# Kernel tuning notes

Hardware: AMD Instinct MI355X
Metric: run time of the kernel (lower is better)

The kernel has to match this reference:

```python
import jax, jax.numpy as jnp
import numpy as np

EMBED = 1024
HEADS = 16
HEAD_DIM = EMBED // HEADS


def setup_inputs() -> dict:
    key = jax.random.key(0)
    ks = jax.random.split(key, 8)
    N, S = 4, 2048
    scale = 1.0 / np.sqrt(HEAD_DIM)
    return {
        "values": jax.random.normal(ks[0], (N, S, EMBED), jnp.float32),
        "keys": jax.random.normal(ks[1], (N, S, EMBED), jnp.float32),
        "query": jax.random.normal(ks[2], (N, S, EMBED), jnp.float32),
        "Wv": jax.random.normal(ks[3], (HEAD_DIM, HEAD_DIM), jnp.float32) * scale,
        "Wk": jax.random.normal(ks[4], (HEAD_DIM, HEAD_DIM), jnp.float32) * scale,
        "Wq": jax.random.normal(ks[5], (HEAD_DIM, HEAD_DIM), jnp.float32) * scale,
        "Wo": jax.random.normal(ks[6], (EMBED, EMBED), jnp.float32) / np.sqrt(EMBED),
        "bo": jax.random.normal(ks[7], (EMBED,), jnp.float32) * 0.01,
    }


def reference(values, keys, query, Wv, Wk, Wq, Wo, bo):
    N = query.shape[0]
    # reshape to [N, S, H, D]
    v = values.reshape(N, -1, HEADS, HEAD_DIM)
    k = keys.reshape(N, -1, HEADS, HEAD_DIM)
    q = query.reshape(N, -1, HEADS, HEAD_DIM)
    # per-head linear projections (torch Linear: x @ W.T)
    v = jnp.einsum("nshd,ed->nshe", v, Wv)
    k = jnp.einsum("nshd,ed->nshe", k, Wk)
    q = jnp.einsum("nshd,ed->nshe", q, Wq)
    # full attention matrix [N, H, Q, K]; note scale uses embed_size**0.5 as in source
    energy = jnp.einsum("nqhd,nkhd->nhqk", q, k)
    attn = jax.nn.softmax(energy / jnp.sqrt(jnp.asarray(EMBED, energy.dtype)), axis=3)
    out = jnp.einsum("nhql,nlhd->nqhd", attn, v).reshape(N, -1, EMBED)
    return out @ Wo.T + bo
```

## Files before the change

### kernel.cpp

```cpp
#include <hip/hip_runtime.h>
#include <hip/hip_bf16.h>

#define EMBED 1024
#define HEADS 16
#define HD    64
#define NB    4
#define SEQ   2048

typedef __bf16 bf16x2 __attribute__((ext_vector_type(2)));
typedef __bf16 bf16x8 __attribute__((ext_vector_type(8)));
typedef float  f32x4  __attribute__((ext_vector_type(4)));
typedef float  f32x16 __attribute__((ext_vector_type(16)));
typedef unsigned uint2v __attribute__((ext_vector_type(2)));

__device__ __forceinline__ unsigned short f2bf(float f) {
    union { float f; unsigned u; } v; v.f = f;
    unsigned r = v.u + 0x7fffu + ((v.u >> 16) & 1u);
    return (unsigned short)(r >> 16);
}
__device__ __forceinline__ unsigned pack2(float a, float b) {
#if __has_builtin(__builtin_amdgcn_cvt_pk_bf16_f32)
    union { bf16x2 v; unsigned u; } c;
    c.v = __builtin_amdgcn_cvt_pk_bf16_f32(a, b);
    return c.u;
#else
    return (unsigned)f2bf(a) | ((unsigned)f2bf(b) << 16);
#endif
}

__global__ __launch_bounds__(256) void cvt_kernel(const float* __restrict__ src,
                                                  unsigned* __restrict__ dst) {
    int i = blockIdx.x * 256 + threadIdx.x;
    float4 v = ((const float4*)src)[i];
    uint2 o;
    o.x = pack2(v.x, v.y);
    o.y = pack2(v.z, v.w);
    ((uint2*)dst)[i] = o;
}

__global__ __launch_bounds__(256) void proj_kernel(
    const float* __restrict__ xq, const float* __restrict__ xk, const float* __restrict__ xv,
    const float* __restrict__ Wq, const float* __restrict__ Wk, const float* __restrict__ Wv,
    unsigned short* __restrict__ Qp, unsigned short* __restrict__ Kp, unsigned short* __restrict__ Vt)
{
    __shared__ __align__(16) unsigned short Wl[64 * 72];
    __shared__ __align__(16) unsigned short Xl[256 * 72];

    int bx = blockIdx.x;
    int p  = bx >> 9;
    int r  = bx & 511;
    int st = r & 7, h = (r >> 3) & 15, n = r >> 7;
    int s0 = st * 256;

    const float* x = (p == 0) ? xq : (p == 1) ? xk : xv;
    const float* W = (p == 0) ? Wq : (p == 1) ? Wk : Wv;
    const float sc = (p == 0) ? 0.045084220027780106f : 1.0f;

    int tid = threadIdx.x;

    for (int i = 0; i < 4; ++i) {
        int idx = tid + i * 256;
        int row = idx >> 4, c4 = idx & 15;
        float4 wv = ((const float4*)W)[row * 16 + c4];
        uint2 pw;
        pw.x = pack2(wv.x, wv.y);
        pw.y = pack2(wv.z, wv.w);
        *(uint2*)&Wl[row * 72 + c4 * 4] = pw;
    }
    const float* xbase = x + (size_t)(n * SEQ + s0) * EMBED + h * HD;
    for (int i = 0; i < 16; ++i) {
        int idx = tid + i * 256;
        int row = idx >> 4, c4 = idx & 15;
        float4 v = *(const float4*)(xbase + (size_t)row * EMBED + c4 * 4);
        uint2 px;
        px.x = pack2(v.x, v.y);
        px.y = pack2(v.z, v.w);
        *(uint2*)&Xl[row * 72 + c4 * 4] = px;
    }
    __syncthreads();

    int w = tid >> 6, lane = tid & 63, ln = lane & 15, qd = lane >> 4;

    bf16x8 a[4][2], b[4][2];
#pragma unroll
    for (int mt = 0; mt < 4; ++mt)
#pragma unroll
        for (int kt = 0; kt < 2; ++kt)
            a[mt][kt] = *(const bf16x8*)&Xl[(w * 64 + mt * 16 + ln) * 72 + kt * 32 + qd * 8];
#pragma unroll
    for (int i = 0; i < 4; ++i)
#pragma unroll
        for (int kt = 0; kt < 2; ++kt)
            b[i][kt] = *(const bf16x8*)&Wl[(i * 16 + ln) * 72 + kt * 32 + qd * 8];

    f32x4 acc[4][4];
    const f32x4 fz = {0.f, 0.f, 0.f, 0.f};
#pragma unroll
    for (int i = 0; i < 4; ++i)
#pragma unroll
        for (int j = 0; j < 4; ++j) acc[i][j] = fz;

    if (p < 2) {
#pragma unroll
        for (int i = 0; i < 4; ++i)
#pragma unroll
            for (int j = 0; j < 4; ++j) {
                acc[i][j] = __builtin_amdgcn_mfma_f32_16x16x32_bf16(b[i][0], a[j][0], acc[i][j], 0, 0, 0);
                acc[i][j] = __builtin_amdgcn_mfma_f32_16x16x32_bf16(b[i][1], a[j][1], acc[i][j], 0, 0, 0);
            }
#pragma unroll
        for (int i = 0; i < 4; ++i)
#pragma unroll
            for (int j = 0; j < 4; ++j) {
                uint2 pk;
                pk.x = pack2(acc[i][j][0] * sc, acc[i][j][1] * sc);
                pk.y = pack2(acc[i][j][2] * sc, acc[i][j][3] * sc);
                *(uint2*)&Xl[(w * 64 + j * 16 + ln) * 72 + i * 16 + qd * 4] = pk;
            }
        __syncthreads();
        unsigned short* outp = (p == 0 ? Qp : Kp) + (size_t)(n * HEADS + h) * SEQ * HD + (size_t)s0 * HD;
        for (int i = 0; i < 8; ++i) {
            int idx = tid + i * 256;
            int row = idx >> 3, ch = idx & 7;
            *(uint4*)(outp + (size_t)row * HD + ch * 8) = *(const uint4*)&Xl[row * 72 + ch * 8];
        }
    } else {
#pragma unroll
        for (int mt = 0; mt < 4; ++mt)
#pragma unroll
            for (int i = 0; i < 4; ++i) {
                acc[mt][i] = __builtin_amdgcn_mfma_f32_16x16x32_bf16(a[mt][0], b[i][0], acc[mt][i], 0, 0, 0);
                acc[mt][i] = __builtin_amdgcn_mfma_f32_16x16x32_bf16(a[mt][1], b[i][1], acc[mt][i], 0, 0, 0);
            }
        __syncthreads();
#pragma unroll
        for (int mt = 0; mt < 4; ++mt)
#pragma unroll
            for (int i = 0; i < 4; ++i) {
                uint2 pk;
                pk.x = pack2(acc[mt][i][0], acc[mt][i][1]);
                pk.y = pack2(acc[mt][i][2], acc[mt][i][3]);
                *(uint2*)&Xl[(i * 16 + ln) * 264 + w * 64 + mt * 16 + qd * 4] = pk;
            }
        __syncthreads();
        unsigned short* outp = Vt + (size_t)(n * HEADS + h) * HD * SEQ + s0;
        for (int i = 0; i < 8; ++i) {
            int idx = tid + i * 256;
            int row = idx >> 5, ch = idx & 31;
            *(uint4*)(outp + (size_t)row * SEQ + ch * 8) = *(const uint4*)&Xl[row * 264 + ch * 8];
        }
    }
}

__global__ __launch_bounds__(512, 4) void attn_kernel(
    const unsigned short* __restrict__ Qp, const unsigned short* __restrict__ Kp,
    const unsigned short* __restrict__ Vt, unsigned short* __restrict__ Xattn)
{
    __shared__ __align__(16) unsigned short SMEM[18432];
    unsigned short* Kl = SMEM;
    unsigned short* Vl = SMEM + 9216;

    int bx = blockIdx.x;
    int head = bx >> 3, qt = bx & 7;
    int n = head >> 4, h16 = head & 15;
    int q0 = qt * 256;

    int tid = threadIdx.x;
    int w = tid >> 6, lane = tid & 63;
    int qc = lane & 31, hh = lane >> 5;

    const unsigned short* Qb = Qp + (size_t)head * SEQ * HD;
    const unsigned short* Kb = Kp + (size_t)head * SEQ * HD;
    const unsigned short* Vb = Vt + (size_t)head * HD * SEQ;

    bf16x8 qb[4];
    {
        int qrow = q0 + w * 32 + qc;
#pragma unroll
        for (int kk = 0; kk < 4; ++kk)
            qb[kk] = *(const bf16x8*)(Qb + (size_t)qrow * HD + kk * 16 + hh * 8);
    }

    f32x16 ot0, ot1;
#pragma unroll
    for (int i = 0; i < 16; ++i) { ot0[i] = 0.f; ot1[i] = 0.f; }
    float ls[4] = {0.f, 0.f, 0.f, 0.f};

    int srow = tid >> 3, sch = tid & 7;

    uint4 rK, rV;
    rK = *(const uint4*)(Kb + (size_t)srow * HD + sch * 8);
    rV = *(const uint4*)(Vb + (size_t)srow * SEQ + 0 + sch * 8);
    *(uint4*)&Kl[srow * 72 + sch * 8] = rK;
    *(uint4*)&Vl[srow * 72 + sch * 8] = rV;
    rK = *(const uint4*)(Kb + (size_t)(64 + srow) * HD + sch * 8);
    rV = *(const uint4*)(Vb + (size_t)srow * SEQ + 64 + sch * 8);

    for (int kc = 0; kc < SEQ; kc += 64) {
        int cur = (kc >> 6) & 1, nxt = cur ^ 1;
        int curo = cur * 4608;
        __syncthreads();

        unsigned pk[2][8];
#pragma unroll
        for (int kt = 0; kt < 2; ++kt) {
            f32x16 c;
#pragma unroll
            for (int i = 0; i < 16; ++i) c[i] = 0.f;
            __builtin_amdgcn_s_setprio(1);
#pragma unroll
            for (int kk = 0; kk < 4; ++kk) {
                bf16x8 ka = *(const bf16x8*)&Kl[curo + (kt * 32 + qc) * 72 + kk * 16 + hh * 8];
                c = __builtin_amdgcn_mfma_f32_32x32x16_bf16(ka, qb[kk], c, 0, 0, 0);
            }
            __builtin_amdgcn_s_setprio(0);
#pragma unroll
            for (int i = 0; i < 8; ++i) {
                float p0 = __builtin_amdgcn_exp2f(c[2 * i]);
                float p1 = __builtin_amdgcn_exp2f(c[2 * i + 1]);
                ls[i & 3] += p0 + p1;
                pk[kt][i] = pack2(p0, p1);
            }
        }

        if (kc + 64 < SEQ) {
            *(uint4*)&Kl[nxt * 4608 + srow * 72 + sch * 8] = rK;
            *(uint4*)&Vl[nxt * 4608 + srow * 72 + sch * 8] = rV;
            int kn = kc + 128 <= SEQ - 64 ? kc + 128 : SEQ - 64;
            rK = *(const uint4*)(Kb + (size_t)(kn + srow) * HD + sch * 8);
            rV = *(const uint4*)(Vb + (size_t)srow * SEQ + kn + sch * 8);
        }

        __builtin_amdgcn_s_setprio(1);
#pragma unroll
        for (int g = 0; g < 4; ++g) {
            const unsigned* P = pk[g >> 1];
            int base = (g & 1) * 4;
            union { unsigned u[4]; bf16x8 v; } bb;
#if __has_builtin(__builtin_amdgcn_permlane32_swap)
            uint2v r  = __builtin_amdgcn_permlane32_swap(P[base + 0], P[base + 2], false, false);
            uint2v rr = __builtin_amdgcn_permlane32_swap(P[base + 1], P[base + 3], false, false);
            bb.u[0] = r.x;
            bb.u[1] = rr.x;
            bb.u[2] = r.y;
            bb.u[3] = rr.y;
#else
            unsigned s0 = hh ? P[base + 0] : P[base + 2];
            unsigned s1 = hh ? P[base + 1] : P[base + 3];
            unsigned r0 = (unsigned)__shfl_xor((int)s0, 32);
            unsigned r1 = (unsigned)__shfl_xor((int)s1, 32);
            bb.u[0] = hh ? r0 : P[base + 0];
            bb.u[1] = hh ? r1 : P[base + 1];
            bb.u[2] = hh ? P[base + 2] : r0;
            bb.u[3] = hh ? P[base + 3] : r1;
#endif
            bf16x8 va0 = *(const bf16x8*)&Vl[curo + qc * 72 + g * 16 + hh * 8];
            bf16x8 va1 = *(const bf16x8*)&Vl[curo + (32 + qc) * 72 + g * 16 + hh * 8];
            ot0 = __builtin_amdgcn_mfma_f32_32x32x16_bf16(va0, bb.v, ot0, 0, 0, 0);
            ot1 = __builtin_amdgcn_mfma_f32_32x32x16_bf16(va1, bb.v, ot1, 0, 0, 0);
        }
        __builtin_amdgcn_s_setprio(0);
    }

    float lsum = (ls[0] + ls[1]) + (ls[2] + ls[3]);
    lsum += __shfl_xor(lsum, 32);
    float inv = 1.0f / lsum;

    __syncthreads();
    int qlocal = w * 32 + qc;
#pragma unroll
    for (int dt = 0; dt < 2; ++dt) {
        const f32x16& o = dt ? ot1 : ot0;
#pragma unroll
        for (int g = 0; g < 4; ++g) {
            uint2 p;
            p.x = pack2(o[4 * g + 0] * inv, o[4 * g + 1] * inv);
            p.y = pack2(o[4 * g + 2] * inv, o[4 * g + 3] * inv);
            *(uint2*)&SMEM[qlocal * 72 + dt * 32 + g * 8 + hh * 4] = p;
        }
    }
    __syncthreads();
    unsigned short* ob = Xattn + (size_t)(n * SEQ + q0) * EMBED + h16 * HD;
#pragma unroll
    for (int i = 0; i < 4; ++i) {
        int idx = tid + i * 512;
        int row = idx >> 3, ch = idx & 7;
        *(uint4*)(ob + (size_t)row * EMBED + ch * 8) = *(const uint4*)&SMEM[row * 72 + ch * 8];
    }
}

__global__ __launch_bounds__(256, 4) void outproj_kernel(
    const unsigned short* __restrict__ X, const unsigned short* __restrict__ Wb,
    const float* __restrict__ bo, float* __restrict__ out)
{
    __shared__ __align__(16) unsigned short Al[64 * 72];
    __shared__ __align__(16) unsigned short Bl[128 * 72];

    int bx = blockIdx.x;
    int cm = bx >> 3, cn = bx & 7;
    int m0 = cm * 64, c0 = cn * 128;
    int tid = threadIdx.x;
    int w = tid >> 6, lane = tid & 63, ln = lane & 15, qd = lane >> 4;
    int chw = w * 32;

    f32x4 acc[4][2];
    const f32x4 fz = {0.f, 0.f, 0.f, 0.f};
#pragma unroll
    for (int mt = 0; mt < 4; ++mt)
#pragma unroll
        for (int nt = 0; nt < 2; ++nt) acc[mt][nt] = fz;

    for (int k0 = 0; k0 < EMBED; k0 += 64) {
        {
#pragma unroll
            for (int i = 0; i < 2; ++i) {
                int idx = tid + i * 256;
                int r2 = idx >> 3, c2 = idx & 7;
                uint4 av = *(const uint4*)(X + (size_t)(m0 + r2) * EMBED + k0 + c2 * 8);
                *(uint4*)&Al[r2 * 72 + c2 * 8] = av;
            }
#pragma unroll
            for (int i = 0; i < 4; ++i) {
                int idx = tid + i * 256;
                int r2 = idx >> 3, c2 = idx & 7;
                uint4 bv = *(const uint4*)(Wb + (size_t)(c0 + r2) * EMBED + k0 + c2 * 8);
                *(uint4*)&Bl[r2 * 72 + c2 * 8] = bv;
            }
        }
        __syncthreads();
        bf16x8 af[4][2], bf_[2][2];
#pragma unroll
        for (int mt = 0; mt < 4; ++mt)
#pragma unroll
            for (int kt = 0; kt < 2; ++kt)
                af[mt][kt] = *(const bf16x8*)&Al[(mt * 16 + ln) * 72 + kt * 32 + qd * 8];
#pragma unroll
        for (int nt = 0; nt < 2; ++nt)
#pragma unroll
            for (int kt = 0; kt < 2; ++kt)
                bf_[nt][kt] = *(const bf16x8*)&Bl[(chw + nt * 16 + ln) * 72 + kt * 32 + qd * 8];
#pragma unroll
        for (int mt = 0; mt < 4; ++mt)
#pragma unroll
            for (int nt = 0; nt < 2; ++nt) {
                acc[mt][nt] = __builtin_amdgcn_mfma_f32_16x16x32_bf16(af[mt][0], bf_[nt][0], acc[mt][nt], 0, 0, 0);
                acc[mt][nt] = __builtin_amdgcn_mfma_f32_16x16x32_bf16(af[mt][1], bf_[nt][1], acc[mt][nt], 0, 0, 0);
            }
        __syncthreads();
    }

#pragma unroll
    for (int nt = 0; nt < 2; ++nt) {
        int col = c0 + chw + nt * 16 + ln;
        float bias = bo[col];
#pragma unroll
        for (int mt = 0; mt < 4; ++mt) {
            int row = m0 + mt * 16 + qd * 4;
#pragma unroll
            for (int rg = 0; rg < 4; ++rg)
                out[(size_t)(row + rg) * EMBED + col] = acc[mt][nt][rg] + bias;
        }
    }
}

extern "C" void kernel_launch(void* const* d_in, const int* in_sizes, int n_in,
                              void* d_out, int out_size, void* d_ws, size_t ws_size,
                              hipStream_t stream) {
    const float* values = (const float*)d_in[0];
    const float* keys   = (const float*)d_in[1];
    const float* query  = (const float*)d_in[2];
    const float* Wv     = (const float*)d_in[3];
    const float* Wk     = (const float*)d_in[4];
    const float* Wq     = (const float*)d_in[5];
    const float* Wo     = (const float*)d_in[6];
    const float* bo     = (const float*)d_in[7];
    float* out = (float*)d_out;

    unsigned short* ws = (unsigned short*)d_ws;
    const size_t HSZ = (size_t)NB * HEADS * SEQ * HD;
    unsigned short* Qp = ws;
    unsigned short* Kp = Qp + HSZ;
    unsigned short* Vt = Kp + HSZ;
    unsigned short* Xa = Vt + HSZ;
    unsigned short* Wb = Xa + HSZ;

    cvt_kernel<<<1024, 256, 0, stream>>>(Wo, (unsigned*)Wb);
    proj_kernel<<<1536, 256, 0, stream>>>(query, keys, values, Wq, Wk, Wv, Qp, Kp, Vt);
    attn_kernel<<<512, 512, 0, stream>>>(Qp, Kp, Vt, Xa);
    outproj_kernel<<<1024, 256, 0, stream>>>(Xa, Wb, bo, out);
}
```

Measured before the change: 264.4 us.

## Software-pipeline attention loop: overlap QK of next tile with PV of previous

Restructures the attention main loop into a three-buffer LDS ring so that the QK^T MFMAs and softmax exp for tile i run in the same iteration as the PV MFMAs for tile i-1. The aim is to let exp/pack work overlap with matrix-core work and to remove the per-tile dependency stall between softmax and PV. It also replaces __syncthreads with a custom barrier that waits only on LDS counters, so in-flight global prefetch loads are not drained at each barrier. LDS grows from 36 KB to 54 KB per block, which may reduce occupancy, and more live registers (two score accumulators plus the packed P fragments) raise register pressure.

```diff
diff --git a/kernel.cpp b/kernel.cpp
--- a/kernel.cpp
+++ b/kernel.cpp
@@ -26,6 +26,12 @@
 #else
     return (unsigned)f2bf(a) | ((unsigned)f2bf(b) << 16);
 #endif
+}
+
+__device__ __forceinline__ void sync_lds() {
+    asm volatile("s_waitcnt lgkmcnt(0)" ::: "memory");
+    __builtin_amdgcn_s_barrier();
+    asm volatile("" ::: "memory");
 }
 
 __global__ __launch_bounds__(256) void cvt_kernel(const float* __restrict__ src,
@@ -156,9 +162,7 @@
     const unsigned short* __restrict__ Qp, const unsigned short* __restrict__ Kp,
     const unsigned short* __restrict__ Vt, unsigned short* __restrict__ Xattn)
 {
-    __shared__ __align__(16) unsigned short SMEM[18432];
-    unsigned short* Kl = SMEM;
-    unsigned short* Vl = SMEM + 9216;
+    __shared__ __align__(16) unsigned short SMEM[27648];
 
     int bx = blockIdx.x;
     int head = bx >> 3, qt = bx & 7;
@@ -187,80 +191,118 @@
     float ls[4] = {0.f, 0.f, 0.f, 0.f};
 
     int srow = tid >> 3, sch = tid & 7;
+    int soff = srow * 72 + sch * 8;
+
+    unsigned pkP[16];
+    f32x16 c0, c1;
+
+#define QK_STEP(KBASE)  do {                                                    \
+    _Pragma("unroll")                                                           \
+    for (int _i = 0; _i < 16; ++_i) { c0[_i] = 0.f; c1[_i] = 0.f; }             \
+    __builtin_amdgcn_s_setprio(1);                                              \
+    _Pragma("unroll")                                                           \
+    for (int kk = 0; kk < 4; ++kk) {                                            \
+        bf16x8 ka = *(const bf16x8*)&SMEM[(KBASE) + qc * 72 + kk * 16 + hh * 8];\
+        c0 = __builtin_amdgcn_mfma_f32_32x32x16_bf16(ka, qb[kk], c0, 0, 0, 0);  \
+    }                                                                           \
+    _Pragma("unroll")                                                           \
+    for (int kk = 0; kk < 4; ++kk) {                                            \
+        bf16x8 ka = *(const bf16x8*)&SMEM[(KBASE) + (32 + qc) * 72 + kk * 16 + hh * 8]; \
+        c1 = __builtin_amdgcn_mfma_f32_32x32x16_bf16(ka, qb[kk], c1, 0, 0, 0);  \
+    }                                                                           \
+    __builtin_amdgcn_s_setprio(0);                                              \
+} while (0)
+
+#define SOFTMAX_STEP() do {                                                     \
+    _Pragma("unroll")                                                           \
+    for (int _i = 0; _i < 8; ++_i) {                                            \
+        float p0 = __builtin_amdgcn_exp2f(c0[2 * _i]);                          \
+        float p1 = __builtin_amdgcn_exp2f(c0[2 * _i + 1]);                      \
+        ls[_i & 3] += p0 + p1;                                                  \
+        pkP[_i] = pack2(p0, p1);                                                \
+    }                                                                           \
+    _Pragma("unroll")                                                           \
+    for (int _i = 0; _i < 8; ++_i) {                                            \
+        float p0 = __builtin_amdgcn_exp2f(c1[2 * _i]);                          \
+        float p1 = __builtin_amdgcn_exp2f(c1[2 * _i + 1]);                      \
+        ls[_i & 3] += p0 + p1;                                                  \
+        pkP[8 + _i] = pack2(p0, p1);                                            \
+    }                                                                           \
+} while (0)
+
+#if __has_builtin(__builtin_amdgcn_permlane32_swap)
+#define PV_FRAG(P, BASE, BB) do {                                               \
+    uint2v r  = __builtin_amdgcn_permlane32_swap((P)[(BASE) + 0], (P)[(BASE) + 2], false, false); \
+    uint2v rr = __builtin_amdgcn_permlane32_swap((P)[(BASE) + 1], (P)[(BASE) + 3], false, false); \
+    BB.u[0] = r.x; BB.u[1] = rr.x; BB.u[2] = r.y; BB.u[3] = rr.y;               \
+} while (0)
+#else
+#define PV_FRAG(P, BASE, BB) do {                                               \
+    unsigned s0_ = hh ? (P)[(BASE) + 0] : (P)[(BASE) + 2];                      \
+    unsigned s1_ = hh ? (P)[(BASE) + 1] : (P)[(BASE) + 3];                      \
+    unsigned r0_ = (unsigned)__shfl_xor((int)s0_, 32);                          \
+    unsigned r1_ = (unsigned)__shfl_xor((int)s1_, 32);                          \
+    BB.u[0] = hh ? r0_ : (P)[(BASE) + 0];                                       \
+    BB.u[1] = hh ? r1_ : (P)[(BASE) + 1];                                       \
+    BB.u[2] = hh ? (P)[(BASE) + 2] : r0_;                                       \
+    BB.u[3] = hh ? (P)[(BASE) + 3] : r1_;                                       \
+} while (0)
+#endif
+
+#define PV_STEP(VBASE) do {                                                     \
+    __builtin_amdgcn_s_setprio(1);                                              \
+    _Pragma("unroll")                                                           \
+    for (int g = 0; g < 4; ++g) {                                               \
+        union { unsigned u[4]; bf16x8 v; } bb;                                  \
+        PV_FRAG(pkP, (g >> 1) * 8 + (g & 1) * 4, bb);                           \
+        bf16x8 va0 = *(const bf16x8*)&SMEM[(VBASE) + qc * 72 + g * 16 + hh * 8];        \
+        bf16x8 va1 = *(const bf16x8*)&SMEM[(VBASE) + (32 + qc) * 72 + g * 16 + hh * 8]; \
+        ot0 = __builtin_amdgcn_mfma_f32_32x32x16_bf16(va0, bb.v, ot0, 0, 0, 0); \
+        ot1 = __builtin_amdgcn_mfma_f32_32x32x16_bf16(va1, bb.v, ot1, 0, 0, 0); \
+    }                                                                           \
+    __builtin_amdgcn_s_setprio(0);                                              \
+} while (0)
 
     uint4 rK, rV;
     rK = *(const uint4*)(Kb + (size_t)srow * HD + sch * 8);
     rV = *(const uint4*)(Vb + (size_t)srow * SEQ + 0 + sch * 8);
-    *(uint4*)&Kl[srow * 72 + sch * 8] = rK;
-    *(uint4*)&Vl[srow * 72 + sch * 8] = rV;
+    *(uint4*)&SMEM[0 + soff] = rK;
+    *(uint4*)&SMEM[4608 + soff] = rV;
     rK = *(const uint4*)(Kb + (size_t)(64 + srow) * HD + sch * 8);
     rV = *(const uint4*)(Vb + (size_t)srow * SEQ + 64 + sch * 8);
 
-    for (int kc = 0; kc < SEQ; kc += 64) {
-        int cur = (kc >> 6) & 1, nxt = cur ^ 1;
-        int curo = cur * 4608;
-        __syncthreads();
-
-        unsigned pk[2][8];
-#pragma unroll
-        for (int kt = 0; kt < 2; ++kt) {
-            f32x16 c;
-#pragma unroll
-            for (int i = 0; i < 16; ++i) c[i] = 0.f;
-            __builtin_amdgcn_s_setprio(1);
-#pragma unroll
-            for (int kk = 0; kk < 4; ++kk) {
-                bf16x8 ka = *(const bf16x8*)&Kl[curo + (kt * 32 + qc) * 72 + kk * 16 + hh * 8];
-                c = __builtin_amdgcn_mfma_f32_32x32x16_bf16(ka, qb[kk], c, 0, 0, 0);
-            }
-            __builtin_amdgcn_s_setprio(0);
-#pragma unroll
-            for (int i = 0; i < 8; ++i) {
-                float p0 = __builtin_amdgcn_exp2f(c[2 * i]);
-                float p1 = __builtin_amdgcn_exp2f(c[2 * i + 1]);
-                ls[i & 3] += p0 + p1;
-                pk[kt][i] = pack2(p0, p1);
-            }
-        }
-
-        if (kc + 64 < SEQ) {
-            *(uint4*)&Kl[nxt * 4608 + srow * 72 + sch * 8] = rK;
-            *(uint4*)&Vl[nxt * 4608 + srow * 72 + sch * 8] = rV;
-            int kn = kc + 128 <= SEQ - 64 ? kc + 128 : SEQ - 64;
+    sync_lds();
+    QK_STEP(0);
+    *(uint4*)&SMEM[9216 + soff] = rK;
+    *(uint4*)&SMEM[9216 + 4608 + soff] = rV;
+    rK = *(const uint4*)(Kb + (size_t)(128 + srow) * HD + sch * 8);
+    rV = *(const uint4*)(Vb + (size_t)srow * SEQ + 128 + sch * 8);
+    SOFTMAX_STEP();
+
+    int b_prv = 0, b_cur = 9216, b_nxt = 18432;
+
+    for (int i = 1; i < 32; ++i) {
+        sync_lds();
+        QK_STEP(b_cur);
+        if (i < 31) {
+            *(uint4*)&SMEM[b_nxt + soff] = rK;
+            *(uint4*)&SMEM[b_nxt + 4608 + soff] = rV;
+        }
+        PV_STEP(b_prv + 4608);
+        if (i < 30) {
+            int kn = (i + 2) * 64;
             rK = *(const uint4*)(Kb + (size_t)(kn + srow) * HD + sch * 8);
             rV = *(const uint4*)(Vb + (size_t)srow * SEQ + kn + sch * 8);
         }
-
-        __builtin_amdgcn_s_setprio(1);
-#pragma unroll
-        for (int g = 0; g < 4; ++g) {
-            const unsigned* P = pk[g >> 1];
-            int base = (g & 1) * 4;
-            union { unsigned u[4]; bf16x8 v; } bb;
-#if __has_builtin(__builtin_amdgcn_permlane32_swap)
-            uint2v r  = __builtin_amdgcn_permlane32_swap(P[base + 0], P[base + 2], false, false);
-            uint2v rr = __builtin_amdgcn_permlane32_swap(P[base + 1], P[base + 3], false, false);
-            bb.u[0] = r.x;
-            bb.u[1] = rr.x;
-            bb.u[2] = r.y;
-            bb.u[3] = rr.y;
-#else
-            unsigned s0 = hh ? P[base + 0] : P[base + 2];
-            unsigned s1 = hh ? P[base + 1] : P[base + 3];
-            unsigned r0 = (unsigned)__shfl_xor((int)s0, 32);
-            unsigned r1 = (unsigned)__shfl_xor((int)s1, 32);
-            bb.u[0] = hh ? r0 : P[base + 0];
-            bb.u[1] = hh ? r1 : P[base + 1];
-            bb.u[2] = hh ? P[base + 2] : r0;
-            bb.u[3] = hh ? P[base + 3] : r1;
-#endif
-            bf16x8 va0 = *(const bf16x8*)&Vl[curo + qc * 72 + g * 16 + hh * 8];
-            bf16x8 va1 = *(const bf16x8*)&Vl[curo + (32 + qc) * 72 + g * 16 + hh * 8];
-            ot0 = __builtin_amdgcn_mfma_f32_32x32x16_bf16(va0, bb.v, ot0, 0, 0, 0);
-            ot1 = __builtin_amdgcn_mfma_f32_32x32x16_bf16(va1, bb.v, ot1, 0, 0, 0);
-        }
-        __builtin_amdgcn_s_setprio(0);
-    }
+        SOFTMAX_STEP();
+        int t = b_prv; b_prv = b_cur; b_cur = b_nxt; b_nxt = t;
+    }
+    PV_STEP(b_prv + 4608);
+
+#undef QK_STEP
+#undef SOFTMAX_STEP
+#undef PV_FRAG
+#undef PV_STEP
 
     float lsum = (ls[0] + ls[1]) + (ls[2] + ls[3]);
     lsum += __shfl_xor(lsum, 32);
```

After: 270.8 us. 2.4% more time.

## Split attention key range across warp pairs with smaller query tiles and swizzled LDS

Applied to the files above, without the earlier changes.

The attention kernel now uses 256-thread blocks covering 64 queries each, four times as many blocks as before. Each pair of warps splits every 64-key chunk between its two members, and the partial outputs and row sums are reduced through shared memory at the end. K/V tiles move to an XOR-swizzled unpadded LDS layout, and the plain syncthreads is replaced by an explicit lgkmcnt wait plus barrier. The aim is better load balance, better occupancy and fewer LDS bank conflicts. The cost is that K/V are reloaded for every block, which means more global traffic, plus an extra cross-warp reduction step.

```diff
diff --git a/kernel.cpp b/kernel.cpp
--- a/kernel.cpp
+++ b/kernel.cpp
@@ -26,6 +26,12 @@
 #else
     return (unsigned)f2bf(a) | ((unsigned)f2bf(b) << 16);
 #endif
+}
+
+__device__ __forceinline__ void sync_lds() {
+    asm volatile("s_waitcnt lgkmcnt(0)" ::: "memory");
+    __builtin_amdgcn_s_barrier();
+    asm volatile("" ::: "memory");
 }
 
 __global__ __launch_bounds__(256) void cvt_kernel(const float* __restrict__ src,
@@ -152,21 +158,20 @@
     }
 }
 
-__global__ __launch_bounds__(512, 4) void attn_kernel(
+__global__ __launch_bounds__(256, 4) void attn_kernel(
     const unsigned short* __restrict__ Qp, const unsigned short* __restrict__ Kp,
     const unsigned short* __restrict__ Vt, unsigned short* __restrict__ Xattn)
 {
-    __shared__ __align__(16) unsigned short SMEM[18432];
-    unsigned short* Kl = SMEM;
-    unsigned short* Vl = SMEM + 9216;
+    __shared__ __align__(16) unsigned short SMEM[16384];
 
     int bx = blockIdx.x;
-    int head = bx >> 3, qt = bx & 7;
+    int head = bx >> 5, qt = bx & 31;
     int n = head >> 4, h16 = head & 15;
-    int q0 = qt * 256;
+    int q0 = qt * 64;
 
     int tid = threadIdx.x;
     int w = tid >> 6, lane = tid & 63;
+    int qi = w >> 1, kh = w & 1;
     int qc = lane & 31, hh = lane >> 5;
 
     const unsigned short* Qb = Qp + (size_t)head * SEQ * HD;
@@ -175,7 +180,7 @@
 
     bf16x8 qb[4];
     {
-        int qrow = q0 + w * 32 + qc;
+        int qrow = q0 + qi * 32 + qc;
 #pragma unroll
         for (int kk = 0; kk < 4; ++kk)
             qb[kk] = *(const bf16x8*)(Qb + (size_t)qrow * HD + kk * 16 + hh * 8);
@@ -186,106 +191,143 @@
     for (int i = 0; i < 16; ++i) { ot0[i] = 0.f; ot1[i] = 0.f; }
     float ls[4] = {0.f, 0.f, 0.f, 0.f};
 
-    int srow = tid >> 3, sch = tid & 7;
-
-    uint4 rK, rV;
-    rK = *(const uint4*)(Kb + (size_t)srow * HD + sch * 8);
-    rV = *(const uint4*)(Vb + (size_t)srow * SEQ + 0 + sch * 8);
-    *(uint4*)&Kl[srow * 72 + sch * 8] = rK;
-    *(uint4*)&Vl[srow * 72 + sch * 8] = rV;
-    rK = *(const uint4*)(Kb + (size_t)(64 + srow) * HD + sch * 8);
-    rV = *(const uint4*)(Vb + (size_t)srow * SEQ + 64 + sch * 8);
-
-    for (int kc = 0; kc < SEQ; kc += 64) {
-        int cur = (kc >> 6) & 1, nxt = cur ^ 1;
-        int curo = cur * 4608;
-        __syncthreads();
-
-        unsigned pk[2][8];
-#pragma unroll
-        for (int kt = 0; kt < 2; ++kt) {
-            f32x16 c;
-#pragma unroll
-            for (int i = 0; i < 16; ++i) c[i] = 0.f;
-            __builtin_amdgcn_s_setprio(1);
-#pragma unroll
-            for (int kk = 0; kk < 4; ++kk) {
-                bf16x8 ka = *(const bf16x8*)&Kl[curo + (kt * 32 + qc) * 72 + kk * 16 + hh * 8];
-                c = __builtin_amdgcn_mfma_f32_32x32x16_bf16(ka, qb[kk], c, 0, 0, 0);
-            }
-            __builtin_amdgcn_s_setprio(0);
-#pragma unroll
-            for (int i = 0; i < 8; ++i) {
-                float p0 = __builtin_amdgcn_exp2f(c[2 * i]);
-                float p1 = __builtin_amdgcn_exp2f(c[2 * i + 1]);
-                ls[i & 3] += p0 + p1;
-                pk[kt][i] = pack2(p0, p1);
-            }
-        }
-
-        if (kc + 64 < SEQ) {
-            *(uint4*)&Kl[nxt * 4608 + srow * 72 + sch * 8] = rK;
-            *(uint4*)&Vl[nxt * 4608 + srow * 72 + sch * 8] = rV;
-            int kn = kc + 128 <= SEQ - 64 ? kc + 128 : SEQ - 64;
-            rK = *(const uint4*)(Kb + (size_t)(kn + srow) * HD + sch * 8);
-            rV = *(const uint4*)(Vb + (size_t)srow * SEQ + kn + sch * 8);
-        }
-
+    int r0 = tid >> 3, scol = tid & 7;
+    int soff = r0 * 64 + (((scol ^ (r0 & 7))) << 3);
+
+    int sw = qc & 7;
+
+    uint4 rK0, rK1, rV0, rV1;
+    rK0 = *(const uint4*)(Kb + (size_t)r0 * HD + scol * 8);
+    rK1 = *(const uint4*)(Kb + (size_t)(r0 + 32) * HD + scol * 8);
+    rV0 = *(const uint4*)(Vb + (size_t)r0 * SEQ + 0 + scol * 8);
+    rV1 = *(const uint4*)(Vb + (size_t)(r0 + 32) * SEQ + 0 + scol * 8);
+    *(uint4*)&SMEM[soff] = rK0;
+    *(uint4*)&SMEM[soff + 2048] = rK1;
+    *(uint4*)&SMEM[8192 + soff] = rV0;
+    *(uint4*)&SMEM[8192 + soff + 2048] = rV1;
+    rK0 = *(const uint4*)(Kb + (size_t)(64 + r0) * HD + scol * 8);
+    rK1 = *(const uint4*)(Kb + (size_t)(96 + r0) * HD + scol * 8);
+    rV0 = *(const uint4*)(Vb + (size_t)r0 * SEQ + 64 + scol * 8);
+    rV1 = *(const uint4*)(Vb + (size_t)(r0 + 32) * SEQ + 64 + scol * 8);
+
+#if __has_builtin(__builtin_amdgcn_permlane32_swap)
+#define PV_FRAG(P, BASE, BB) do {                                               \
+    uint2v r  = __builtin_amdgcn_permlane32_swap((P)[(BASE) + 0], (P)[(BASE) + 2], false, false); \
+    uint2v rr = __builtin_amdgcn_permlane32_swap((P)[(BASE) + 1], (P)[(BASE) + 3], false, false); \
+    BB.u[0] = r.x; BB.u[1] = rr.x; BB.u[2] = r.y; BB.u[3] = rr.y;               \
+} while (0)
+#else
+#define PV_FRAG(P, BASE, BB) do {                                               \
+    unsigned s0_ = hh ? (P)[(BASE) + 0] : (P)[(BASE) + 2];                      \
+    unsigned s1_ = hh ? (P)[(BASE) + 1] : (P)[(BASE) + 3];                      \
+    unsigned r0_ = (unsigned)__shfl_xor((int)s0_, 32);                          \
+    unsigned r1_ = (unsigned)__shfl_xor((int)s1_, 32);                          \
+    BB.u[0] = hh ? r0_ : (P)[(BASE) + 0];                                       \
+    BB.u[1] = hh ? r1_ : (P)[(BASE) + 1];                                       \
+    BB.u[2] = hh ? (P)[(BASE) + 2] : r0_;                                       \
+    BB.u[3] = hh ? (P)[(BASE) + 3] : r1_;                                       \
+} while (0)
+#endif
+
+    int krow = kh * 32 + qc;
+    int kbase_row = krow * 64;
+    int vrow0 = qc * 64, vrow1 = (32 + qc) * 64;
+    int jv = kh * 4 + hh;
+
+    for (int i = 0; i < 32; ++i) {
+        int cb = (i & 1) << 12;
+        int nb = ((i + 1) & 1) << 12;
+        sync_lds();
+
+        f32x16 c;
+#pragma unroll
+        for (int z = 0; z < 16; ++z) c[z] = 0.f;
         __builtin_amdgcn_s_setprio(1);
 #pragma unroll
-        for (int g = 0; g < 4; ++g) {
-            const unsigned* P = pk[g >> 1];
-            int base = (g & 1) * 4;
+        for (int kk = 0; kk < 4; ++kk) {
+            bf16x8 ka = *(const bf16x8*)&SMEM[cb + kbase_row + (((kk * 2 + hh) ^ sw) << 3)];
+            c = __builtin_amdgcn_mfma_f32_32x32x16_bf16(ka, qb[kk], c, 0, 0, 0);
+        }
+        __builtin_amdgcn_s_setprio(0);
+
+        if (i < 31) {
+            *(uint4*)&SMEM[nb + soff] = rK0;
+            *(uint4*)&SMEM[nb + soff + 2048] = rK1;
+            *(uint4*)&SMEM[nb + 8192 + soff] = rV0;
+            *(uint4*)&SMEM[nb + 8192 + soff + 2048] = rV1;
+        }
+
+        unsigned pk[8];
+#pragma unroll
+        for (int z = 0; z < 8; ++z) {
+            float p0 = __builtin_amdgcn_exp2f(c[2 * z]);
+            float p1 = __builtin_amdgcn_exp2f(c[2 * z + 1]);
+            ls[z & 3] += p0 + p1;
+            pk[z] = pack2(p0, p1);
+        }
+
+        if (i < 30) {
+            int kn = (i + 2) * 64;
+            rK0 = *(const uint4*)(Kb + (size_t)(kn + r0) * HD + scol * 8);
+            rK1 = *(const uint4*)(Kb + (size_t)(kn + r0 + 32) * HD + scol * 8);
+            rV0 = *(const uint4*)(Vb + (size_t)r0 * SEQ + kn + scol * 8);
+            rV1 = *(const uint4*)(Vb + (size_t)(r0 + 32) * SEQ + kn + scol * 8);
+        }
+
+        __builtin_amdgcn_s_setprio(1);
+#pragma unroll
+        for (int ks = 0; ks < 2; ++ks) {
             union { unsigned u[4]; bf16x8 v; } bb;
-#if __has_builtin(__builtin_amdgcn_permlane32_swap)
-            uint2v r  = __builtin_amdgcn_permlane32_swap(P[base + 0], P[base + 2], false, false);
-            uint2v rr = __builtin_amdgcn_permlane32_swap(P[base + 1], P[base + 3], false, false);
-            bb.u[0] = r.x;
-            bb.u[1] = rr.x;
-            bb.u[2] = r.y;
-            bb.u[3] = rr.y;
-#else
-            unsigned s0 = hh ? P[base + 0] : P[base + 2];
-            unsigned s1 = hh ? P[base + 1] : P[base + 3];
-            unsigned r0 = (unsigned)__shfl_xor((int)s0, 32);
-            unsigned r1 = (unsigned)__shfl_xor((int)s1, 32);
-            bb.u[0] = hh ? r0 : P[base + 0];
-            bb.u[1] = hh ? r1 : P[base + 1];
-            bb.u[2] = hh ? P[base + 2] : r0;
-            bb.u[3] = hh ? P[base + 3] : r1;
-#endif
-            bf16x8 va0 = *(const bf16x8*)&Vl[curo + qc * 72 + g * 16 + hh * 8];
-            bf16x8 va1 = *(const bf16x8*)&Vl[curo + (32 + qc) * 72 + g * 16 + hh * 8];
+            PV_FRAG(pk, ks * 4, bb);
+            int col = ((jv + ks * 2) ^ sw) << 3;
+            bf16x8 va0 = *(const bf16x8*)&SMEM[8192 + cb + vrow0 + col];
+            bf16x8 va1 = *(const bf16x8*)&SMEM[8192 + cb + vrow1 + col];
             ot0 = __builtin_amdgcn_mfma_f32_32x32x16_bf16(va0, bb.v, ot0, 0, 0, 0);
             ot1 = __builtin_amdgcn_mfma_f32_32x32x16_bf16(va1, bb.v, ot1, 0, 0, 0);
         }
         __builtin_amdgcn_s_setprio(0);
     }
+#undef PV_FRAG
 
     float lsum = (ls[0] + ls[1]) + (ls[2] + ls[3]);
     lsum += __shfl_xor(lsum, 32);
-    float inv = 1.0f / lsum;
 
     __syncthreads();
-    int qlocal = w * 32 + qc;
-#pragma unroll
-    for (int dt = 0; dt < 2; ++dt) {
-        const f32x16& o = dt ? ot1 : ot0;
-#pragma unroll
-        for (int g = 0; g < 4; ++g) {
-            uint2 p;
-            p.x = pack2(o[4 * g + 0] * inv, o[4 * g + 1] * inv);
-            p.y = pack2(o[4 * g + 2] * inv, o[4 * g + 3] * inv);
-            *(uint2*)&SMEM[qlocal * 72 + dt * 32 + g * 8 + hh * 4] = p;
+    float* SF = (float*)SMEM;
+    if (kh == 0) {
+#pragma unroll
+        for (int j = 0; j < 16; ++j) SF[qi * 2048 + j * 64 + lane] = ot0[j];
+#pragma unroll
+        for (int j = 0; j < 16; ++j) SF[qi * 2048 + (16 + j) * 64 + lane] = ot1[j];
+        if (hh == 0) SF[4096 + qi * 32 + qc] = lsum;
+    }
+    __syncthreads();
+    if (kh == 1) {
+#pragma unroll
+        for (int j = 0; j < 16; ++j) ot0[j] += SF[qi * 2048 + j * 64 + lane];
+#pragma unroll
+        for (int j = 0; j < 16; ++j) ot1[j] += SF[qi * 2048 + (16 + j) * 64 + lane];
+        float inv = 1.0f / (lsum + SF[4096 + qi * 32 + qc]);
+        int qlocal = qi * 32 + qc;
+#pragma unroll
+        for (int dt = 0; dt < 2; ++dt) {
+            const f32x16& o = dt ? ot1 : ot0;
+#pragma unroll
+            for (int g = 0; g < 4; ++g) {
+                uint2 p;
+                p.x = pack2(o[4 * g + 0] * inv, o[4 * g + 1] * inv);
+                p.y = pack2(o[4 * g + 2] * inv, o[4 * g + 3] * inv);
+                *(uint2*)&SMEM[8320 + qlocal * 72 + dt * 32 + g * 8 + hh * 4] = p;
+            }
         }
     }
     __syncthreads();
     unsigned short* ob = Xattn + (size_t)(n * SEQ + q0) * EMBED + h16 * HD;
 #pragma unroll
-    for (int i = 0; i < 4; ++i) {
-        int idx = tid + i * 512;
+    for (int i = 0; i < 2; ++i) {
+        int idx = tid + i * 256;
         int row = idx >> 3, ch = idx & 7;
-        *(uint4*)(ob + (size_t)row * EMBED + ch * 8) = *(const uint4*)&SMEM[row * 72 + ch * 8];
+        *(uint4*)(ob + (size_t)row * EMBED + ch * 8) = *(const uint4*)&SMEM[8320 + row * 72 + ch * 8];
     }
 }
 
@@ -386,6 +428,6 @@
 
     cvt_kernel<<<1024, 256, 0, stream>>>(Wo, (unsigned*)Wb);
     proj_kernel<<<1536, 256, 0, stream>>>(query, keys, values, Wq, Wk, Wv, Qp, Kp, Vt);
-    attn_kernel<<<512, 512, 0, stream>>>(Qp, Kp, Vt, Xa);
+    attn_kernel<<<2048, 256, 0, stream>>>(Qp, Kp, Vt, Xa);
     outproj_kernel<<<1024, 256, 0, stream>>>(Xa, Wb, bo, out);
 }
```

After: 290.3 us. 9.8% more time.

## Double-buffer outproj GEMM with 128x128 tiles and reorder attention prefetch

Applied to the files above, without the earlier changes.

The output-projection GEMM moves to 512-thread blocks computing 128x128 tiles, with double-buffered LDS and register prefetch two k-steps ahead. A lighter LDS-only barrier replaces the two __syncthreads per iteration. This is meant to hide global-load latency and halve B-tile reloads, at the cost of more LDS per block and lower occupancy. In the attention kernel, the next-tile LDS stores and global prefetch now come before the QK MFMAs, and the s_setprio hints are removed.

```diff
diff --git a/kernel.cpp b/kernel.cpp
--- a/kernel.cpp
+++ b/kernel.cpp
@@ -26,6 +26,12 @@
 #else
     return (unsigned)f2bf(a) | ((unsigned)f2bf(b) << 16);
 #endif
+}
+
+__device__ __forceinline__ void sync_lds() {
+    asm volatile("s_waitcnt lgkmcnt(0)" ::: "memory");
+    __builtin_amdgcn_s_barrier();
+    asm volatile("" ::: "memory");
 }
 
 __global__ __launch_bounds__(256) void cvt_kernel(const float* __restrict__ src,
@@ -201,28 +207,6 @@
         int curo = cur * 4608;
         __syncthreads();
 
-        unsigned pk[2][8];
-#pragma unroll
-        for (int kt = 0; kt < 2; ++kt) {
-            f32x16 c;
-#pragma unroll
-            for (int i = 0; i < 16; ++i) c[i] = 0.f;
-            __builtin_amdgcn_s_setprio(1);
-#pragma unroll
-            for (int kk = 0; kk < 4; ++kk) {
-                bf16x8 ka = *(const bf16x8*)&Kl[curo + (kt * 32 + qc) * 72 + kk * 16 + hh * 8];
-                c = __builtin_amdgcn_mfma_f32_32x32x16_bf16(ka, qb[kk], c, 0, 0, 0);
-            }
-            __builtin_amdgcn_s_setprio(0);
-#pragma unroll
-            for (int i = 0; i < 8; ++i) {
-                float p0 = __builtin_amdgcn_exp2f(c[2 * i]);
-                float p1 = __builtin_amdgcn_exp2f(c[2 * i + 1]);
-                ls[i & 3] += p0 + p1;
-                pk[kt][i] = pack2(p0, p1);
-            }
-        }
-
         if (kc + 64 < SEQ) {
             *(uint4*)&Kl[nxt * 4608 + srow * 72 + sch * 8] = rK;
             *(uint4*)&Vl[nxt * 4608 + srow * 72 + sch * 8] = rV;
@@ -231,7 +215,26 @@
             rV = *(const uint4*)(Vb + (size_t)srow * SEQ + kn + sch * 8);
         }
 
-        __builtin_amdgcn_s_setprio(1);
+        unsigned pk[2][8];
+#pragma unroll
+        for (int kt = 0; kt < 2; ++kt) {
+            f32x16 c;
+#pragma unroll
+            for (int i = 0; i < 16; ++i) c[i] = 0.f;
+#pragma unroll
+            for (int kk = 0; kk < 4; ++kk) {
+                bf16x8 ka = *(const bf16x8*)&Kl[curo + (kt * 32 + qc) * 72 + kk * 16 + hh * 8];
+                c = __builtin_amdgcn_mfma_f32_32x32x16_bf16(ka, qb[kk], c, 0, 0, 0);
+            }
+#pragma unroll
+            for (int i = 0; i < 8; ++i) {
+                float p0 = __builtin_amdgcn_exp2f(c[2 * i]);
+                float p1 = __builtin_amdgcn_exp2f(c[2 * i + 1]);
+                ls[i & 3] += p0 + p1;
+                pk[kt][i] = pack2(p0, p1);
+            }
+        }
+
 #pragma unroll
         for (int g = 0; g < 4; ++g) {
             const unsigned* P = pk[g >> 1];
@@ -259,7 +262,6 @@
             ot0 = __builtin_amdgcn_mfma_f32_32x32x16_bf16(va0, bb.v, ot0, 0, 0, 0);
             ot1 = __builtin_amdgcn_mfma_f32_32x32x16_bf16(va1, bb.v, ot1, 0, 0, 0);
         }
-        __builtin_amdgcn_s_setprio(0);
     }
 
     float lsum = (ls[0] + ls[1]) + (ls[2] + ls[3]);
@@ -289,19 +291,25 @@
     }
 }
 
-__global__ __launch_bounds__(256, 4) void outproj_kernel(
+__global__ __launch_bounds__(512, 2) void outproj_kernel(
     const unsigned short* __restrict__ X, const unsigned short* __restrict__ Wb,
     const float* __restrict__ bo, float* __restrict__ out)
 {
-    __shared__ __align__(16) unsigned short Al[64 * 72];
-    __shared__ __align__(16) unsigned short Bl[128 * 72];
+    __shared__ __align__(16) unsigned short Al[2][128 * 72];
+    __shared__ __align__(16) unsigned short Bl[2][128 * 72];
 
     int bx = blockIdx.x;
     int cm = bx >> 3, cn = bx & 7;
-    int m0 = cm * 64, c0 = cn * 128;
+    int m0 = cm * 128, c0 = cn * 128;
     int tid = threadIdx.x;
     int w = tid >> 6, lane = tid & 63, ln = lane & 15, qd = lane >> 4;
-    int chw = w * 32;
+    int wr = w >> 2, wc = w & 3;
+
+    int r1 = tid >> 3, ch = tid & 7;
+    int o1 = r1 * 72 + ch * 8;
+    int o2 = (r1 + 64) * 72 + ch * 8;
+    const unsigned short* Xb = X + (size_t)(m0 + r1) * EMBED + ch * 8;
+    const unsigned short* Wbb = Wb + (size_t)(c0 + r1) * EMBED + ch * 8;
 
     f32x4 acc[4][2];
     const f32x4 fz = {0.f, 0.f, 0.f, 0.f};
@@ -310,35 +318,49 @@
 #pragma unroll
         for (int nt = 0; nt < 2; ++nt) acc[mt][nt] = fz;
 
-    for (int k0 = 0; k0 < EMBED; k0 += 64) {
-        {
-#pragma unroll
-            for (int i = 0; i < 2; ++i) {
-                int idx = tid + i * 256;
-                int r2 = idx >> 3, c2 = idx & 7;
-                uint4 av = *(const uint4*)(X + (size_t)(m0 + r2) * EMBED + k0 + c2 * 8);
-                *(uint4*)&Al[r2 * 72 + c2 * 8] = av;
-            }
-#pragma unroll
-            for (int i = 0; i < 4; ++i) {
-                int idx = tid + i * 256;
-                int r2 = idx >> 3, c2 = idx & 7;
-                uint4 bv = *(const uint4*)(Wb + (size_t)(c0 + r2) * EMBED + k0 + c2 * 8);
-                *(uint4*)&Bl[r2 * 72 + c2 * 8] = bv;
-            }
-        }
-        __syncthreads();
+    uint4 a0, a1, b0, b1;
+    a0 = *(const uint4*)(Xb);
+    a1 = *(const uint4*)(Xb + (size_t)64 * EMBED);
+    b0 = *(const uint4*)(Wbb);
+    b1 = *(const uint4*)(Wbb + (size_t)64 * EMBED);
+    *(uint4*)&Al[0][o1] = a0;
+    *(uint4*)&Al[0][o2] = a1;
+    *(uint4*)&Bl[0][o1] = b0;
+    *(uint4*)&Bl[0][o2] = b1;
+    a0 = *(const uint4*)(Xb + 64);
+    a1 = *(const uint4*)(Xb + (size_t)64 * EMBED + 64);
+    b0 = *(const uint4*)(Wbb + 64);
+    b1 = *(const uint4*)(Wbb + (size_t)64 * EMBED + 64);
+
+    for (int i = 0; i < 16; ++i) {
+        int cur = i & 1, nxt = cur ^ 1;
+        sync_lds();
+
+        if (i < 15) {
+            *(uint4*)&Al[nxt][o1] = a0;
+            *(uint4*)&Al[nxt][o2] = a1;
+            *(uint4*)&Bl[nxt][o1] = b0;
+            *(uint4*)&Bl[nxt][o2] = b1;
+        }
+        if (i < 14) {
+            int k0 = (i + 2) * 64;
+            a0 = *(const uint4*)(Xb + k0);
+            a1 = *(const uint4*)(Xb + (size_t)64 * EMBED + k0);
+            b0 = *(const uint4*)(Wbb + k0);
+            b1 = *(const uint4*)(Wbb + (size_t)64 * EMBED + k0);
+        }
+
         bf16x8 af[4][2], bf_[2][2];
 #pragma unroll
         for (int mt = 0; mt < 4; ++mt)
 #pragma unroll
             for (int kt = 0; kt < 2; ++kt)
-                af[mt][kt] = *(const bf16x8*)&Al[(mt * 16 + ln) * 72 + kt * 32 + qd * 8];
+                af[mt][kt] = *(const bf16x8*)&Al[cur][(wr * 64 + mt * 16 + ln) * 72 + kt * 32 + qd * 8];
 #pragma unroll
         for (int nt = 0; nt < 2; ++nt)
 #pragma unroll
             for (int kt = 0; kt < 2; ++kt)
-                bf_[nt][kt] = *(const bf16x8*)&Bl[(chw + nt * 16 + ln) * 72 + kt * 32 + qd * 8];
+                bf_[nt][kt] = *(const bf16x8*)&Bl[cur][(wc * 32 + nt * 16 + ln) * 72 + kt * 32 + qd * 8];
 #pragma unroll
         for (int mt = 0; mt < 4; ++mt)
 #pragma unroll
@@ -346,16 +368,15 @@
                 acc[mt][nt] = __builtin_amdgcn_mfma_f32_16x16x32_bf16(af[mt][0], bf_[nt][0], acc[mt][nt], 0, 0, 0);
                 acc[mt][nt] = __builtin_amdgcn_mfma_f32_16x16x32_bf16(af[mt][1], bf_[nt][1], acc[mt][nt], 0, 0, 0);
             }
-        __syncthreads();
     }
 
 #pragma unroll
     for (int nt = 0; nt < 2; ++nt) {
-        int col = c0 + chw + nt * 16 + ln;
+        int col = c0 + wc * 32 + nt * 16 + ln;
         float bias = bo[col];
 #pragma unroll
         for (int mt = 0; mt < 4; ++mt) {
-            int row = m0 + mt * 16 + qd * 4;
+            int row = m0 + wr * 64 + mt * 16 + qd * 4;
 #pragma unroll
             for (int rg = 0; rg < 4; ++rg)
                 out[(size_t)(row + rg) * EMBED + col] = acc[mt][nt][rg] + bias;
@@ -387,5 +408,5 @@
     cvt_kernel<<<1024, 256, 0, stream>>>(Wo, (unsigned*)Wb);
     proj_kernel<<<1536, 256, 0, stream>>>(query, keys, values, Wq, Wk, Wv, Qp, Kp, Vt);
     attn_kernel<<<512, 512, 0, stream>>>(Qp, Kp, Vt, Xa);
-    outproj_kernel<<<1024, 256, 0, stream>>>(Xa, Wb, bo, out);
-}
+    outproj_kernel<<<512, 512, 0, stream>>>(Xa, Wb, bo, out);
+}
```

After: 271.4 us. 1.03x slower.
